# Kernel optimization log

Measured on AMD Instinct MI355X. Metric: run time of the kernel, lower is better.

The kernel has to match this reference:

```python
import jax, jax.numpy as jnp
import numpy as np

B, S, E, H = 2, 2048, 1024, 16
HD = E // H  # head_dim = 64
NEG = jnp.float32(-1e9)


def setup_inputs() -> dict:
    key = jax.random.key(0)
    k1, k2, k3 = jax.random.split(key, 3)
    x = jax.random.normal(k1, (B, S, E), dtype=jnp.float32)
    w_qkv = jax.random.normal(k2, (E, 3 * E), dtype=jnp.float32) * 0.02
    b_qkv = jnp.zeros((3 * E,), dtype=jnp.float32)
    w_proj = jax.random.normal(k3, (E, E), dtype=jnp.float32) * 0.02
    b_proj = jnp.zeros((E,), dtype=jnp.float32)
    return {"x": x, "w_qkv": w_qkv, "b_qkv": b_qkv, "w_proj": w_proj, "b_proj": b_proj}


def reference(x, w_qkv, b_qkv, w_proj, b_proj):
    # c_attn (GPT2 Conv1D): x @ W + b -> [B,S,3E]
    qkv = x @ w_qkv + b_qkv
    q, k, v = jnp.split(qkv, 3, axis=-1)
    # split heads -> [B,H,S,HD]
    def heads(t):
        return t.reshape(B, S, H, HD).transpose(0, 2, 1, 3)
    q, k, v = heads(q), heads(k), heads(v)
    # scaled QK^T, causal mask, softmax (attn_pdrop=0 so dropout is identity)
    scores = jnp.einsum("bhqd,bhkd->bhqk", q, k) / jnp.sqrt(jnp.float32(HD))
    causal = jnp.tril(jnp.ones((S, S), dtype=bool))
    scores = jnp.where(causal, scores, NEG)
    attn = jax.nn.softmax(scores, axis=-1)
    out = jnp.einsum("bhqk,bhkd->bhqd", attn, v)
    out = out.transpose(0, 2, 1, 3).reshape(B, S, E)
    # c_proj
    return out @ w_proj + b_proj
```

## Files before the change

### kernel.cpp

```cpp
#include <hip/hip_runtime.h>


typedef __bf16 bf16;
typedef __bf16 bf16x4 __attribute__((ext_vector_type(4)));
typedef __bf16 bf16x8 __attribute__((ext_vector_type(8)));
typedef float f32x4 __attribute__((ext_vector_type(4)));

#define GLOBAL_AS(p) ((const __attribute__((address_space(1))) void*)(p))
#define LDS_AS(p) ((__attribute__((address_space(3))) void*)(p))

__device__ __forceinline__ void g2l16(const void* g, void* l) {
  __builtin_amdgcn_global_load_lds(GLOBAL_AS(g), LDS_AS(l), 16, 0, 0);
}

__global__ __launch_bounds__(256) void cast_bf16_kernel(
    const float* __restrict__ X, bf16* __restrict__ Y) {
  const int i = (blockIdx.x * 256 + threadIdx.x) * 4;
  const float4 v = *(const float4*)(X + i);
  bf16x4 o;
  o.x = (bf16)v.x; o.y = (bf16)v.y; o.z = (bf16)v.z; o.w = (bf16)v.w;
  *(bf16x4*)(Y + i) = o;
}

__global__ __launch_bounds__(256) void transpose_cast_kernel(
    const float* __restrict__ W, bf16* __restrict__ Wt, int R, int C) {
  __shared__ float tile[32][33];
  const int c0 = blockIdx.x * 32, r0 = blockIdx.y * 32;
  const int tx = threadIdx.x, ty = threadIdx.y;
#pragma unroll
  for (int i = ty; i < 32; i += 8) tile[i][tx] = W[(r0 + i) * C + c0 + tx];
  __syncthreads();
#pragma unroll
  for (int i = ty; i < 32; i += 8)
    Wt[(c0 + i) * R + r0 + tx] = (bf16)tile[tx][i];
}

template <int N, int EPI>
__global__ __launch_bounds__(256) void gemm_bt_kernel(
    const bf16* __restrict__ A, const bf16* __restrict__ Bt,
    const float* __restrict__ bias, float* __restrict__ Cf,
    bf16* __restrict__ Qo, bf16* __restrict__ Ko, bf16* __restrict__ Vo) {
  constexpr int K = 1024;
  __shared__ bf16 As[128 * 32];
  __shared__ bf16 Bs[128 * 32];
  const int t = threadIdx.x;
  const int m0 = blockIdx.x * 128;
  const int n0 = blockIdx.y * 128;
  const int wave = t >> 6, lane = t & 63;
  const int wr = (wave >> 1) * 64, wc = (wave & 1) * 64;
  const int lr = lane & 15, lg = lane >> 4;
  f32x4 acc[4][4] = {};
  const bf16* ag = A + (m0 + (t >> 2)) * K + (t & 3) * 8;
  const bf16* bg = Bt + (n0 + (t >> 2)) * K + (t & 3) * 8;
  for (int k0 = 0; k0 < K; k0 += 32) {
    __syncthreads();
    g2l16(ag, &As[t * 8]);
    g2l16(ag + 64 * K, &As[2048 + t * 8]);
    g2l16(bg, &Bs[t * 8]);
    g2l16(bg + 64 * K, &Bs[2048 + t * 8]);
    ag += 32; bg += 32;
    __syncthreads();
    bf16x8 af[4], bfr[4];
#pragma unroll
    for (int i = 0; i < 4; i++)
      af[i] = *(const bf16x8*)&As[(wr + i * 16 + lr) * 32 + lg * 8];
#pragma unroll
    for (int j = 0; j < 4; j++)
      bfr[j] = *(const bf16x8*)&Bs[(wc + j * 16 + lr) * 32 + lg * 8];
#pragma unroll
    for (int i = 0; i < 4; i++)
#pragma unroll
      for (int j = 0; j < 4; j++)
        acc[i][j] = __builtin_amdgcn_mfma_f32_16x16x32_bf16(af[i], bfr[j],
                                                            acc[i][j], 0, 0, 0);
  }
#pragma unroll
  for (int i = 0; i < 4; i++) {
#pragma unroll
    for (int j = 0; j < 4; j++) {
      const int n = n0 + wc + j * 16 + lr;
      const float bv = bias[n];
#pragma unroll
      for (int r = 0; r < 4; r++) {
        const int m = m0 + wr + i * 16 + lg * 4 + r;
        const float v = acc[i][j][r] + bv;
        if (EPI == 0) {
          Cf[m * N + n] = v;
        } else {
          const int b = m >> 11, s = m & 2047;
          const int reg = n >> 10, e = n & 1023;
          const int h = e >> 6, d = e & 63;
          bf16* dst = (reg == 0) ? Qo : (reg == 1) ? Ko : Vo;
          dst[((b * 16 + h) * 2048 + s) * 64 + d] = (bf16)v;
        }
      }
    }
  }
}

__global__ __launch_bounds__(256) void vtrans_kernel(
    const bf16* __restrict__ V, bf16* __restrict__ Vt) {
  __shared__ bf16 tile[64][72];
  const int t = threadIdx.x;
  const int bh = blockIdx.y;
  const int s0 = blockIdx.x * 64;
#pragma unroll
  for (int i = 0; i < 2; i++) {
    const int u = i * 256 + t;
    const int s = u >> 3, c = u & 7;
    *(bf16x8*)&tile[s][c * 8] =
        *(const bf16x8*)(V + ((size_t)bh * 2048 + s0 + s) * 64 + c * 8);
  }
  __syncthreads();
  {
    const int d = t >> 2, part = t & 3;
    bf16x8 o0, o1;
#pragma unroll
    for (int e = 0; e < 8; e++) {
      o0[e] = tile[part * 16 + e][d];
      o1[e] = tile[part * 16 + 8 + e][d];
    }
    bf16* dst = Vt + ((size_t)bh * 64 + d) * 2048 + s0 + part * 16;
    *(bf16x8*)dst = o0;
    *(bf16x8*)(dst + 8) = o1;
  }
}

__device__ __forceinline__ void stage_kv(const bf16* __restrict__ Kg,
                                         const bf16* __restrict__ Vg, int kb,
                                         bf16* ks, bf16* vs, int t) {
  int u = t, r = u >> 3, c = (u & 7) ^ (r & 7);
  g2l16(Kg + (kb + r) * 64 + c * 8, ks + u * 8);
  g2l16(Vg + r * 2048 + kb + c * 8, vs + u * 8);
  u = 256 + t; r = u >> 3; c = (u & 7) ^ (r & 7);
  g2l16(Kg + (kb + r) * 64 + c * 8, ks + u * 8);
  g2l16(Vg + r * 2048 + kb + c * 8, vs + u * 8);
}

__global__ __launch_bounds__(256, 3) void attn_kernel(
    const bf16* __restrict__ Qb, const bf16* __restrict__ Kb,
    const bf16* __restrict__ Vt, bf16* __restrict__ Obf) {
  __shared__ bf16 Ks[2][64 * 64];
  __shared__ bf16 Vs[2][64 * 64];
  __shared__ bf16 Ps[4][16 * 72];
  const int t = threadIdx.x;
  const int w = t >> 6, lane = t & 63;
  const int lr = lane & 15, lg = lane >> 4;
  const int bx = blockIdx.x;
  const int xcd = bx & 7, idx = bx >> 3;
  const int bh = (idx & 3) * 8 + xcd;
  const int strip = 31 - (idx >> 2);
  const int qb = strip * 64 + w * 16;
  const bf16* Qg = Qb + (size_t)bh * 2048 * 64;
  const bf16* Kg = Kb + (size_t)bh * 2048 * 64;
  const bf16* Vg = Vt + (size_t)bh * 64 * 2048;
  bf16x8 bq[2];
#pragma unroll
  for (int h = 0; h < 2; h++)
    bq[h] = *(const bf16x8*)(Qg + (qb + lr) * 64 + h * 32 + lg * 8);
  f32x4 oacc[4] = {};
  float mrow = -1e30f, lrow = 0.f;
  const float SCL = 0.18033688f;
  bf16* ps = &Ps[w][0];
  const int T = strip + 1;
  stage_kv(Kg, Vg, 0, Ks[0], Vs[0], t);
  for (int ti = 0; ti < T; ++ti) {
    __syncthreads();
    if (ti + 1 < T) stage_kv(Kg, Vg, (ti + 1) * 64, Ks[(ti + 1) & 1],
                             Vs[(ti + 1) & 1], t);
    const int kb = ti * 64;
    const bf16* ks = Ks[ti & 1];
    const bf16* vs = Vs[ti & 1];
    bf16x8 ak[4][2], av[4][2];
#pragma unroll
    for (int j = 0; j < 4; j++) {
      const int row = j * 16 + lr;
#pragma unroll
      for (int h = 0; h < 2; h++)
        ak[j][h] =
            *(const bf16x8*)(ks + (row * 8 + ((h * 4 + lg) ^ (row & 7))) * 8);
    }
#pragma unroll
    for (int dt = 0; dt < 4; dt++) {
      const int row = dt * 16 + lr;
#pragma unroll
      for (int h = 0; h < 2; h++)
        av[dt][h] =
            *(const bf16x8*)(vs + (row * 8 + ((h * 4 + lg) ^ (row & 7))) * 8);
    }
    f32x4 sacc[4];
#pragma unroll
    for (int j = 0; j < 4; j++) {
      f32x4 s = {};
      s = __builtin_amdgcn_mfma_f32_16x16x32_bf16(ak[j][0], bq[0], s, 0, 0, 0);
      s = __builtin_amdgcn_mfma_f32_16x16x32_bf16(ak[j][1], bq[1], s, 0, 0, 0);
      sacc[j] = s;
    }
    float p[4][4];
#pragma unroll
    for (int j = 0; j < 4; j++)
#pragma unroll
      for (int r = 0; r < 4; r++) p[j][r] = sacc[j][r] * SCL;
    if (kb + 63 > qb) {
      const int q = qb + lr;
#pragma unroll
      for (int j = 0; j < 4; j++)
#pragma unroll
        for (int r = 0; r < 4; r++)
          if (kb + j * 16 + lg * 4 + r > q) p[j][r] = -1e30f;
    }
    float tm = -1e30f;
#pragma unroll
    for (int j = 0; j < 4; j++)
#pragma unroll
      for (int r = 0; r < 4; r++) tm = fmaxf(tm, p[j][r]);
    tm = fmaxf(tm, __shfl_xor(tm, 16, 64));
    tm = fmaxf(tm, __shfl_xor(tm, 32, 64));
    const float mnew = fmaxf(mrow, tm);
    const float alpha = exp2f(mrow - mnew);
    mrow = mnew;
    float rs = 0.f;
    bf16x4 pk[4];
#pragma unroll
    for (int j = 0; j < 4; j++)
#pragma unroll
      for (int r = 0; r < 4; r++) {
        const float e = exp2f(p[j][r] - mnew);
        rs += e;
        pk[j][r] = (bf16)e;
      }
    rs += __shfl_xor(rs, 16, 64);
    rs += __shfl_xor(rs, 32, 64);
    lrow = lrow * alpha + rs;
    asm volatile("" ::: "memory");
#pragma unroll
    for (int j = 0; j < 4; j++)
      *(bf16x4*)(ps + lr * 72 + j * 16 + lg * 4) = pk[j];
    asm volatile("s_waitcnt lgkmcnt(0)" ::: "memory");
    bf16x8 bp[2];
#pragma unroll
    for (int h = 0; h < 2; h++)
      bp[h] = *(const bf16x8*)(ps + lr * 72 + h * 32 + lg * 8);
#pragma unroll
    for (int dt = 0; dt < 4; dt++) {
      f32x4 o = oacc[dt];
#pragma unroll
      for (int r = 0; r < 4; r++) o[r] *= alpha;
      o = __builtin_amdgcn_mfma_f32_16x16x32_bf16(av[dt][0], bp[0], o, 0, 0, 0);
      o = __builtin_amdgcn_mfma_f32_16x16x32_bf16(av[dt][1], bp[1], o, 0, 0, 0);
      oacc[dt] = o;
    }
  }
  const int b = bh >> 4, hh = bh & 15;
  const int q = qb + lr;
  const float inv = 1.0f / lrow;
  bf16* orow = Obf + ((size_t)(b * 2048 + q)) * 1024 + hh * 64;
#pragma unroll
  for (int dt = 0; dt < 4; dt++) {
    bf16x4 ov;
#pragma unroll
    for (int r = 0; r < 4; r++) ov[r] = (bf16)(oacc[dt][r] * inv);
    *(bf16x4*)(orow + dt * 16 + lg * 4) = ov;
  }
}

extern "C" void kernel_launch(void* const* d_in, const int* in_sizes, int n_in,
                              void* d_out, int out_size, void* d_ws,
                              size_t ws_size, hipStream_t stream) {
  const float* x      = (const float*)d_in[0];
  const float* w_qkv  = (const float*)d_in[1];
  const float* b_qkv  = (const float*)d_in[2];
  const float* w_proj = (const float*)d_in[3];
  const float* b_proj = (const float*)d_in[4];
  float* out = (float*)d_out;

  char* w = (char*)d_ws;
  bf16* Xbf = (bf16*)w;  w += 4096 * 1024 * 2;
  bf16* Wqt = (bf16*)w;  w += 3072 * 1024 * 2;
  bf16* Wpt = (bf16*)w;  w += 1024 * 1024 * 2;
  bf16* Qb  = (bf16*)w;  w += 2 * 16 * 2048 * 64 * 2;
  bf16* Kb  = (bf16*)w;  w += 2 * 16 * 2048 * 64 * 2;
  bf16* Vb  = (bf16*)w;  w += 2 * 16 * 2048 * 64 * 2;
  bf16* Obf = (bf16*)w;  w += 4096 * 1024 * 2;
  bf16* Vt  = Xbf;

  cast_bf16_kernel<<<4096, 256, 0, stream>>>(x, Xbf);
  transpose_cast_kernel<<<dim3(96, 32), dim3(32, 8), 0, stream>>>(w_qkv, Wqt, 1024, 3072);
  transpose_cast_kernel<<<dim3(32, 32), dim3(32, 8), 0, stream>>>(w_proj, Wpt, 1024, 1024);
  gemm_bt_kernel<3072, 1><<<dim3(32, 24), 256, 0, stream>>>(
      Xbf, Wqt, b_qkv, nullptr, Qb, Kb, Vb);
  vtrans_kernel<<<dim3(32, 32), 256, 0, stream>>>(Vb, Vt);
  attn_kernel<<<1024, 256, 0, stream>>>(Qb, Kb, Vt, Obf);
  gemm_bt_kernel<1024, 0><<<dim3(32, 8), 256, 0, stream>>>(
      Obf, Wpt, b_proj, out, nullptr, nullptr, nullptr);
}
```

Baseline: 193.2 us.

## Double attention query tile per wave, fuse prep kernels, fold softmax scale into Q

The attention kernel now gives each wave 32 query rows (two 16-row groups) instead of 16, so each staged K/V tile is reused across twice as many queries. The block count is halved to 512 and the occupancy hint drops to 2 blocks per CU. The KV loop is unrolled by two with fixed double buffers and a per-wave causal bound. The softmax scale moves into the QKV GEMM epilogue, and the three cast/transpose prep kernels merge into one launch. The costs are higher register pressure, lower occupancy and fewer blocks to balance the causal triangle.

Result: no change. 190.9 us (-1.2%).

```diff
diff --git a/kernel.cpp b/kernel.cpp
--- a/kernel.cpp
+++ b/kernel.cpp
@@ -13,26 +13,39 @@
   __builtin_amdgcn_global_load_lds(GLOBAL_AS(g), LDS_AS(l), 16, 0, 0);
 }
 
-__global__ __launch_bounds__(256) void cast_bf16_kernel(
-    const float* __restrict__ X, bf16* __restrict__ Y) {
-  const int i = (blockIdx.x * 256 + threadIdx.x) * 4;
-  const float4 v = *(const float4*)(X + i);
-  bf16x4 o;
-  o.x = (bf16)v.x; o.y = (bf16)v.y; o.z = (bf16)v.z; o.w = (bf16)v.w;
-  *(bf16x4*)(Y + i) = o;
-}
-
-__global__ __launch_bounds__(256) void transpose_cast_kernel(
-    const float* __restrict__ W, bf16* __restrict__ Wt, int R, int C) {
+#define QSCL 0.18033688f
+
+__global__ __launch_bounds__(256) void prep_kernel(
+    const float* __restrict__ x, const float* __restrict__ wq,
+    const float* __restrict__ wp, bf16* __restrict__ Xbf,
+    bf16* __restrict__ Wqt, bf16* __restrict__ Wpt) {
   __shared__ float tile[32][33];
-  const int c0 = blockIdx.x * 32, r0 = blockIdx.y * 32;
-  const int tx = threadIdx.x, ty = threadIdx.y;
+  const int t = threadIdx.x;
+  const int b = blockIdx.x;
+  if (b < 4096) {
+    const int i = (b * 256 + t) * 4;
+    const float4 v = *(const float4*)(x + i);
+    bf16x4 o;
+    o.x = (bf16)v.x; o.y = (bf16)v.y; o.z = (bf16)v.z; o.w = (bf16)v.w;
+    *(bf16x4*)(Xbf + i) = o;
+    return;
+  }
+  const float* W; bf16* Wt; int C, bx, by;
+  if (b < 7168) {
+    const int b2 = b - 4096;
+    W = wq; Wt = Wqt; C = 3072; bx = b2 % 96; by = b2 / 96;
+  } else {
+    const int b3 = b - 7168;
+    W = wp; Wt = Wpt; C = 1024; bx = b3 & 31; by = b3 >> 5;
+  }
+  const int c0 = bx * 32, r0 = by * 32;
+  const int tx = t & 31, ty = t >> 5;
 #pragma unroll
   for (int i = ty; i < 32; i += 8) tile[i][tx] = W[(r0 + i) * C + c0 + tx];
   __syncthreads();
 #pragma unroll
   for (int i = ty; i < 32; i += 8)
-    Wt[(c0 + i) * R + r0 + tx] = (bf16)tile[tx][i];
+    Wt[(c0 + i) * 1024 + r0 + tx] = (bf16)tile[tx][i];
 }
 
 template <int N, int EPI>
@@ -91,7 +104,8 @@
           const int reg = n >> 10, e = n & 1023;
           const int h = e >> 6, d = e & 63;
           bf16* dst = (reg == 0) ? Qo : (reg == 1) ? Ko : Vo;
-          dst[((b * 16 + h) * 2048 + s) * 64 + d] = (bf16)v;
+          const float vv = (reg == 0) ? v * QSCL : v;
+          dst[((b * 16 + h) * 2048 + s) * 64 + d] = (bf16)vv;
         }
       }
     }
@@ -137,7 +151,98 @@
   g2l16(Vg + r * 2048 + kb + c * 8, vs + u * 8);
 }
 
-__global__ __launch_bounds__(256, 3) void attn_kernel(
+__device__ __forceinline__ void attn_compute(
+    const bf16* __restrict__ ks, const bf16* __restrict__ vs, int kb, int lr,
+    int lg, int qb, const bf16x8 (&bq)[2][2], bf16* ps, f32x4 (&oacc)[2][4],
+    float (&mreg)[2], float (&lreg)[2]) {
+  bf16x8 ak[4][2], av[4][2];
+#pragma unroll
+  for (int j = 0; j < 4; j++) {
+    const int row = j * 16 + lr;
+#pragma unroll
+    for (int h = 0; h < 2; h++)
+      ak[j][h] =
+          *(const bf16x8*)(ks + (row * 8 + ((h * 4 + lg) ^ (row & 7))) * 8);
+  }
+#pragma unroll
+  for (int dt = 0; dt < 4; dt++) {
+    const int row = dt * 16 + lr;
+#pragma unroll
+    for (int h = 0; h < 2; h++)
+      av[dt][h] =
+          *(const bf16x8*)(vs + (row * 8 + ((h * 4 + lg) ^ (row & 7))) * 8);
+  }
+  f32x4 sacc[2][4];
+#pragma unroll
+  for (int g = 0; g < 2; g++)
+#pragma unroll
+    for (int j = 0; j < 4; j++) {
+      f32x4 s = {};
+      s = __builtin_amdgcn_mfma_f32_16x16x32_bf16(ak[j][0], bq[g][0], s, 0, 0, 0);
+      s = __builtin_amdgcn_mfma_f32_16x16x32_bf16(ak[j][1], bq[g][1], s, 0, 0, 0);
+      sacc[g][j] = s;
+    }
+#pragma unroll
+  for (int g = 0; g < 2; g++) {
+    const int qg0 = qb + g * 16;
+    float p[4][4];
+#pragma unroll
+    for (int j = 0; j < 4; j++)
+#pragma unroll
+      for (int r = 0; r < 4; r++) p[j][r] = sacc[g][j][r];
+    if (kb + 63 > qg0) {
+      const int q = qg0 + lr;
+#pragma unroll
+      for (int j = 0; j < 4; j++)
+#pragma unroll
+        for (int r = 0; r < 4; r++)
+          if (kb + j * 16 + lg * 4 + r > q) p[j][r] = -1e30f;
+    }
+    float tm = -1e30f;
+#pragma unroll
+    for (int j = 0; j < 4; j++)
+#pragma unroll
+      for (int r = 0; r < 4; r++) tm = fmaxf(tm, p[j][r]);
+    tm = fmaxf(tm, __shfl_xor(tm, 16, 64));
+    tm = fmaxf(tm, __shfl_xor(tm, 32, 64));
+    const float mnew = fmaxf(mreg[g], tm);
+    const float alpha = __builtin_amdgcn_exp2f(mreg[g] - mnew);
+    mreg[g] = mnew;
+    float rs = 0.f;
+    bf16x4 pk[4];
+#pragma unroll
+    for (int j = 0; j < 4; j++)
+#pragma unroll
+      for (int r = 0; r < 4; r++) {
+        const float e = __builtin_amdgcn_exp2f(p[j][r] - mnew);
+        rs += e;
+        pk[j][r] = (bf16)e;
+      }
+    rs += __shfl_xor(rs, 16, 64);
+    rs += __shfl_xor(rs, 32, 64);
+    lreg[g] = lreg[g] * alpha + rs;
+    asm volatile("" ::: "memory");
+#pragma unroll
+    for (int j = 0; j < 4; j++)
+      *(bf16x4*)(ps + lr * 72 + j * 16 + lg * 4) = pk[j];
+    asm volatile("s_waitcnt lgkmcnt(0)" ::: "memory");
+    bf16x8 bp[2];
+#pragma unroll
+    for (int h = 0; h < 2; h++)
+      bp[h] = *(const bf16x8*)(ps + lr * 72 + h * 32 + lg * 8);
+#pragma unroll
+    for (int dt = 0; dt < 4; dt++) {
+      f32x4 o = oacc[g][dt];
+#pragma unroll
+      for (int r = 0; r < 4; r++) o[r] *= alpha;
+      o = __builtin_amdgcn_mfma_f32_16x16x32_bf16(av[dt][0], bp[0], o, 0, 0, 0);
+      o = __builtin_amdgcn_mfma_f32_16x16x32_bf16(av[dt][1], bp[1], o, 0, 0, 0);
+      oacc[g][dt] = o;
+    }
+  }
+}
+
+__global__ __launch_bounds__(256, 2) void attn_kernel(
     const bf16* __restrict__ Qb, const bf16* __restrict__ Kb,
     const bf16* __restrict__ Vt, bf16* __restrict__ Obf) {
   __shared__ bf16 Ks[2][64 * 64];
@@ -149,118 +254,49 @@
   const int bx = blockIdx.x;
   const int xcd = bx & 7, idx = bx >> 3;
   const int bh = (idx & 3) * 8 + xcd;
-  const int strip = 31 - (idx >> 2);
-  const int qb = strip * 64 + w * 16;
+  const int strip = 15 - (idx >> 2);
+  const int qb = strip * 128 + w * 32;
   const bf16* Qg = Qb + (size_t)bh * 2048 * 64;
   const bf16* Kg = Kb + (size_t)bh * 2048 * 64;
   const bf16* Vg = Vt + (size_t)bh * 64 * 2048;
-  bf16x8 bq[2];
-#pragma unroll
-  for (int h = 0; h < 2; h++)
-    bq[h] = *(const bf16x8*)(Qg + (qb + lr) * 64 + h * 32 + lg * 8);
-  f32x4 oacc[4] = {};
-  float mrow = -1e30f, lrow = 0.f;
-  const float SCL = 0.18033688f;
+  bf16x8 bq[2][2];
+#pragma unroll
+  for (int g = 0; g < 2; g++)
+#pragma unroll
+    for (int h = 0; h < 2; h++)
+      bq[g][h] =
+          *(const bf16x8*)(Qg + (qb + g * 16 + lr) * 64 + h * 32 + lg * 8);
+  f32x4 oacc[2][4] = {};
+  float mreg[2] = {-1e30f, -1e30f};
+  float lreg[2] = {0.f, 0.f};
   bf16* ps = &Ps[w][0];
-  const int T = strip + 1;
+  const int T = 2 * strip + 2;
+  const int Tw = 2 * strip + 1 + (w >> 1);
   stage_kv(Kg, Vg, 0, Ks[0], Vs[0], t);
-  for (int ti = 0; ti < T; ++ti) {
+  for (int ti = 0; ti + 2 <= T; ti += 2) {
     __syncthreads();
-    if (ti + 1 < T) stage_kv(Kg, Vg, (ti + 1) * 64, Ks[(ti + 1) & 1],
-                             Vs[(ti + 1) & 1], t);
-    const int kb = ti * 64;
-    const bf16* ks = Ks[ti & 1];
-    const bf16* vs = Vs[ti & 1];
-    bf16x8 ak[4][2], av[4][2];
-#pragma unroll
-    for (int j = 0; j < 4; j++) {
-      const int row = j * 16 + lr;
-#pragma unroll
-      for (int h = 0; h < 2; h++)
-        ak[j][h] =
-            *(const bf16x8*)(ks + (row * 8 + ((h * 4 + lg) ^ (row & 7))) * 8);
-    }
+    stage_kv(Kg, Vg, (ti + 1) * 64, Ks[1], Vs[1], t);
+    if (ti < Tw)
+      attn_compute(Ks[0], Vs[0], ti * 64, lr, lg, qb, bq, ps, oacc, mreg, lreg);
+    __syncthreads();
+    if (ti + 2 < T) stage_kv(Kg, Vg, (ti + 2) * 64, Ks[0], Vs[0], t);
+    if (ti + 1 < Tw)
+      attn_compute(Ks[1], Vs[1], (ti + 1) * 64, lr, lg, qb, bq, ps, oacc, mreg,
+                   lreg);
+  }
+  const int b = bh >> 4, hh = bh & 15;
+#pragma unroll
+  for (int g = 0; g < 2; g++) {
+    const int q = qb + g * 16 + lr;
+    const float inv = 1.0f / lreg[g];
+    bf16* orow = Obf + ((size_t)(b * 2048 + q)) * 1024 + hh * 64;
 #pragma unroll
     for (int dt = 0; dt < 4; dt++) {
-      const int row = dt * 16 + lr;
-#pragma unroll
-      for (int h = 0; h < 2; h++)
-        av[dt][h] =
-            *(const bf16x8*)(vs + (row * 8 + ((h * 4 + lg) ^ (row & 7))) * 8);
-    }
-    f32x4 sacc[4];
-#pragma unroll
-    for (int j = 0; j < 4; j++) {
-      f32x4 s = {};
-      s = __builtin_amdgcn_mfma_f32_16x16x32_bf16(ak[j][0], bq[0], s, 0, 0, 0);
-      s = __builtin_amdgcn_mfma_f32_16x16x32_bf16(ak[j][1], bq[1], s, 0, 0, 0);
-      sacc[j] = s;
-    }
-    float p[4][4];
-#pragma unroll
-    for (int j = 0; j < 4; j++)
-#pragma unroll
-      for (int r = 0; r < 4; r++) p[j][r] = sacc[j][r] * SCL;
-    if (kb + 63 > qb) {
-      const int q = qb + lr;
-#pragma unroll
-      for (int j = 0; j < 4; j++)
-#pragma unroll
-        for (int r = 0; r < 4; r++)
-          if (kb + j * 16 + lg * 4 + r > q) p[j][r] = -1e30f;
-    }
-    float tm = -1e30f;
-#pragma unroll
-    for (int j = 0; j < 4; j++)
-#pragma unroll
-      for (int r = 0; r < 4; r++) tm = fmaxf(tm, p[j][r]);
-    tm = fmaxf(tm, __shfl_xor(tm, 16, 64));
-    tm = fmaxf(tm, __shfl_xor(tm, 32, 64));
-    const float mnew = fmaxf(mrow, tm);
-    const float alpha = exp2f(mrow - mnew);
-    mrow = mnew;
-    float rs = 0.f;
-    bf16x4 pk[4];
-#pragma unroll
-    for (int j = 0; j < 4; j++)
-#pragma unroll
-      for (int r = 0; r < 4; r++) {
-        const float e = exp2f(p[j][r] - mnew);
-        rs += e;
-        pk[j][r] = (bf16)e;
-      }
-    rs += __shfl_xor(rs, 16, 64);
-    rs += __shfl_xor(rs, 32, 64);
-    lrow = lrow * alpha + rs;
-    asm volatile("" ::: "memory");
-#pragma unroll
-    for (int j = 0; j < 4; j++)
-      *(bf16x4*)(ps + lr * 72 + j * 16 + lg * 4) = pk[j];
-    asm volatile("s_waitcnt lgkmcnt(0)" ::: "memory");
-    bf16x8 bp[2];
-#pragma unroll
-    for (int h = 0; h < 2; h++)
-      bp[h] = *(const bf16x8*)(ps + lr * 72 + h * 32 + lg * 8);
-#pragma unroll
-    for (int dt = 0; dt < 4; dt++) {
-      f32x4 o = oacc[dt];
-#pragma unroll
-      for (int r = 0; r < 4; r++) o[r] *= alpha;
-      o = __builtin_amdgcn_mfma_f32_16x16x32_bf16(av[dt][0], bp[0], o, 0, 0, 0);
-      o = __builtin_amdgcn_mfma_f32_16x16x32_bf16(av[dt][1], bp[1], o, 0, 0, 0);
-      oacc[dt] = o;
-    }
-  }
-  const int b = bh >> 4, hh = bh & 15;
-  const int q = qb + lr;
-  const float inv = 1.0f / lrow;
-  bf16* orow = Obf + ((size_t)(b * 2048 + q)) * 1024 + hh * 64;
-#pragma unroll
-  for (int dt = 0; dt < 4; dt++) {
-    bf16x4 ov;
-#pragma unroll
-    for (int r = 0; r < 4; r++) ov[r] = (bf16)(oacc[dt][r] * inv);
-    *(bf16x4*)(orow + dt * 16 + lg * 4) = ov;
+      bf16x4 ov;
+#pragma unroll
+      for (int r = 0; r < 4; r++) ov[r] = (bf16)(oacc[g][dt][r] * inv);
+      *(bf16x4*)(orow + dt * 16 + lg * 4) = ov;
+    }
   }
 }
 
@@ -284,13 +320,11 @@
   bf16* Obf = (bf16*)w;  w += 4096 * 1024 * 2;
   bf16* Vt  = Xbf;
 
-  cast_bf16_kernel<<<4096, 256, 0, stream>>>(x, Xbf);
-  transpose_cast_kernel<<<dim3(96, 32), dim3(32, 8), 0, stream>>>(w_qkv, Wqt, 1024, 3072);
-  transpose_cast_kernel<<<dim3(32, 32), dim3(32, 8), 0, stream>>>(w_proj, Wpt, 1024, 1024);
+  prep_kernel<<<8192, 256, 0, stream>>>(x, w_qkv, w_proj, Xbf, Wqt, Wpt);
   gemm_bt_kernel<3072, 1><<<dim3(32, 24), 256, 0, stream>>>(
       Xbf, Wqt, b_qkv, nullptr, Qb, Kb, Vb);
   vtrans_kernel<<<dim3(32, 32), 256, 0, stream>>>(Vb, Vt);
-  attn_kernel<<<1024, 256, 0, stream>>>(Qb, Kb, Vt, Obf);
+  attn_kernel<<<512, 256, 0, stream>>>(Qb, Kb, Vt, Obf);
   gemm_bt_kernel<1024, 0><<<dim3(32, 8), 256, 0, stream>>>(
       Obf, Wpt, b_proj, out, nullptr, nullptr, nullptr);
 }
```
